# Kernel tuning notes

Hardware: AMD Instinct MI355X
Metric: run time of the kernel (lower is better)

## Reference

```python
import jax, jax.numpy as jnp
import numpy as np

N = 50000   # nodes
E = 600000  # edges (avg degree 12)
F = 16      # raw node features
P = 32      # n_channels_preproc
C = 128     # n_channels
L = 6       # n_gnn_layers
LBL = 2     # n_labels


def _dense_init(k, fan_in, shape):
    return (jax.random.normal(k, shape, jnp.float32) / np.float32(np.sqrt(fan_in)))


def setup_inputs() -> dict:
    key = jax.random.key(0)
    ks = jax.random.split(key, 12)
    return {
        "x": jax.random.normal(ks[0], (N, F), jnp.float32),
        "edge_src": jax.random.randint(ks[1], (E,), 0, N, dtype=jnp.int32),
        "edge_dst": jax.random.randint(ks[2], (E,), 0, N, dtype=jnp.int32),
        "edge_weight": jax.random.uniform(ks[3], (E,), jnp.float32),  # normalized-adjacency values
        "preproc_W": _dense_init(ks[4], F, (F, P)), "preproc_b": jnp.zeros((P,), jnp.float32),
        "fc_in1_W": _dense_init(ks[5], P, (P, C)), "fc_in1_b": jnp.zeros((C,), jnp.float32),
        "fc_in2_W": _dense_init(ks[6], P, (P, C)), "fc_in2_b": jnp.zeros((C,), jnp.float32),
        "gcn_W": _dense_init(ks[7], C, (L, C, C)), "gcn_b": jnp.zeros((L, C), jnp.float32),
        "fcg_W": _dense_init(ks[8], 2 * C, (L, 2 * C, C)), "fcg_b": jnp.zeros((L, C), jnp.float32),
        "last1_W": _dense_init(ks[9], 2 * C, (2 * C, C)), "last1_b": jnp.zeros((C,), jnp.float32),
        "last2_W": _dense_init(ks[10], C, (C, LBL)), "last2_b": jnp.zeros((LBL,), jnp.float32),
    }


def reference(x, edge_src, edge_dst, edge_weight,
              preproc_W, preproc_b, fc_in1_W, fc_in1_b, fc_in2_W, fc_in2_b,
              gcn_W, gcn_b, fcg_W, fcg_b, last1_W, last1_b, last2_W, last2_b):
    relu = jax.nn.relu
    h = relu(x @ preproc_W + preproc_b)                      # preproc Dense
    node_id = relu(h @ fc_in1_W + fc_in1_b)                  # node identity branch
    h = relu(h @ fc_in2_W + fc_in2_b)

    def layer(h, params):
        W, b, Wf, bf = params
        # GCNConv: act(A_hat @ (h @ W) + b), A_hat as COO edge list
        hw = h @ W                                           # [N, C]
        msg = hw[edge_src] * edge_weight[:, None]            # [E, C]
        agg = jax.ops.segment_sum(msg, edge_dst, num_segments=N)
        g = relu(agg + b)
        merged = jnp.concatenate([node_id, g], axis=-1)      # [N, 2C]
        return relu(merged @ Wf + bf), None                  # dropout = identity (eval)

    h, _ = jax.lax.scan(layer, h, (gcn_W, gcn_b, fcg_W, fcg_b))

    merged = jnp.concatenate([node_id, h], axis=-1)
    h = relu(merged @ last1_W + last1_b)
    return jax.nn.sigmoid(h @ last2_W + last2_b)             # [N, n_labels]
```

## Files before the change

### kernel.cpp

```cpp
#include <hip/hip_runtime.h>
#include <cstddef>
#include <cstdint>

#define NN 50000
#define NE 600000
#define NB 391

typedef __attribute__((ext_vector_type(8))) short bf16x8;
typedef __attribute__((ext_vector_type(4))) float f32x4;

#define SWZ(x) (((x) ^ ((x) >> 2)) & 3)

#define GLDS16(src, dst)                                                     \
    __builtin_amdgcn_global_load_lds(                                        \
        (const __attribute__((address_space(1))) void*)(src),                \
        (__attribute__((address_space(3))) void*)(dst), 16, 0, 0)

__device__ __forceinline__ float bf2f(ushort u) {
    return __uint_as_float(((uint32_t)u) << 16);
}
__device__ __forceinline__ ushort f2bf(float f) {
    uint32_t b = __float_as_uint(f);
    return (ushort)((b + 0x7FFF + ((b >> 16) & 1)) >> 16);
}

__global__ __launch_bounds__(256)
void convbh_kernel(const float* __restrict__ f1W, const float* __restrict__ f2W,
                   const float* __restrict__ gW, const float* __restrict__ fgW,
                   const float* __restrict__ l1W, ushort* __restrict__ wt,
                   const int* __restrict__ dst, int* __restrict__ bcnt)
{
    if (blockIdx.x < 1312) {
        int i = blockIdx.x * 256 + threadIdx.x;
        if (i >= 335872) return;
        float v;
        if (i < 4096) {
            int c = i >> 5, k = i & 31;
            v = f1W[k * 128 + c];
        } else if (i < 8192) {
            int j = i - 4096; int c = j >> 5, k = j & 31;
            v = f2W[k * 128 + c];
        } else if (i < 8192 + 98304) {
            int j = i - 8192; int l = j >> 14, r = j & 16383;
            int c = r >> 7, k = r & 127;
            v = gW[l * 16384 + k * 128 + c];
        } else if (i < 8192 + 98304 + 196608) {
            int j = i - (8192 + 98304); int l = j >> 15, r = j & 32767;
            int c = r >> 8, k = r & 255;
            v = fgW[l * 32768 + k * 128 + c];
        } else {
            int j = i - (8192 + 98304 + 196608);
            int c = j >> 8, k = j & 255;
            v = l1W[k * 128 + c];
        }
        wt[i] = f2bf(v);
    } else {
        __shared__ int h[NB];
        int tx = threadIdx.x;
        for (int i = tx; i < NB; i += 256) h[i] = 0;
        __syncthreads();
        int e0 = (blockIdx.x - 1312) * 1024;
#pragma unroll
        for (int k = 0; k < 4; ++k) {
            int e = e0 + k * 256 + tx;
            if (e < NE) atomicAdd(&h[dst[e] >> 7], 1);
        }
        __syncthreads();
        for (int i = tx; i < NB; i += 256)
            if (h[i]) atomicAdd(&bcnt[i], h[i]);
    }
}

__global__ __launch_bounds__(512)
void bscan_kernel(const int* __restrict__ bcnt, int* __restrict__ bbase,
                  int* __restrict__ bcur)
{
    __shared__ int buf[512];
    int t = threadIdx.x;
    int v = (t < NB) ? bcnt[t] : 0;
    buf[t] = v;
    __syncthreads();
    for (int s = 1; s < 512; s <<= 1) {
        int u = (t >= s) ? buf[t - s] : 0;
        __syncthreads();
        buf[t] += u;
        __syncthreads();
    }
    if (t < NB) {
        int ex = buf[t] - v;
        bbase[t] = ex;
        bcur[t]  = ex;
    }
    if (t == 0) bbase[NB] = NE;
}

__global__ __launch_bounds__(256)
void pass1_kernel(const int* __restrict__ src, const int* __restrict__ dst,
                  const float* __restrict__ w, int* __restrict__ bcur,
                  unsigned int* __restrict__ stage_pk,
                  unsigned char* __restrict__ stage_dl)
{
    __shared__ int cnt[NB];
    __shared__ int gbase[NB];
    int tx = threadIdx.x;
    for (int i = tx; i < NB; i += 256) cnt[i] = 0;
    __syncthreads();
    int e0 = blockIdx.x * 1024;
    int myd[4], myrank[4];
    unsigned int mypk[4];
#pragma unroll
    for (int k = 0; k < 4; ++k) {
        int e = e0 + k * 256 + tx;
        if (e < NE) {
            int d = dst[e];
            myd[k]    = d;
            mypk[k]   = (unsigned int)src[e] | ((unsigned int)f2bf(w[e]) << 17);
            myrank[k] = atomicAdd(&cnt[d >> 7], 1);
        } else {
            myd[k] = -1;
        }
    }
    __syncthreads();
    for (int i = tx; i < NB; i += 256)
        gbase[i] = cnt[i] ? atomicAdd(&bcur[i], cnt[i]) : 0;
    __syncthreads();
#pragma unroll
    for (int k = 0; k < 4; ++k) {
        if (myd[k] >= 0) {
            int p = gbase[myd[k] >> 7] + myrank[k];
            stage_pk[p] = mypk[k];
            stage_dl[p] = (unsigned char)(myd[k] & 127);
        }
    }
}

__global__ __launch_bounds__(256)
void p2pre_kernel(const unsigned int* __restrict__ stage_pk,
                  const unsigned char* __restrict__ stage_dl,
                  const int* __restrict__ bbase,
                  unsigned int* __restrict__ esw, int* __restrict__ off,
                  const float* __restrict__ x, const float* __restrict__ preW,
                  const float* __restrict__ preb, ushort* __restrict__ h0b)
{
    if (blockIdx.x < NB) {
        __shared__ int h[128];
        __shared__ int lofs[128];
        int b    = blockIdx.x;
        int tx   = threadIdx.x;
        int base = bbase[b];
        int cnt  = bbase[b + 1] - base;
        if (tx < 128) h[tx] = 0;
        __syncthreads();
        for (int i = tx; i < cnt; i += 256)
            atomicAdd(&h[stage_dl[base + i]], 1);
        __syncthreads();
        if (tx == 0) {
            int run = 0;
            for (int i = 0; i < 128; ++i) { lofs[i] = run; run += h[i]; }
        }
        __syncthreads();
        int node0 = b * 128;
        if (tx < 128) {
            int n = node0 + tx;
            if (n < NN) off[n] = base + lofs[tx];
            h[tx] = 0;
        }
        if (b == NB - 1 && tx == 0) off[NN] = NE;
        __syncthreads();
        for (int i = tx; i < cnt; i += 256) {
            int d = stage_dl[base + i];
            int r = atomicAdd(&h[d], 1);
            esw[base + lofs[d] + r] = stage_pk[base + i];
        }
    } else {
        __shared__ float Wl[512];
        __shared__ float bl[32];
        int tx = threadIdx.x;
        Wl[tx]       = preW[tx];
        Wl[tx + 256] = preW[tx + 256];
        if (tx < 32) bl[tx] = preb[tx];
        __syncthreads();
        int n = (blockIdx.x - NB) * 256 + tx;
        if (n >= NN) return;
        float xr[16];
        const float4* xp = (const float4*)(x + (size_t)n * 16);
#pragma unroll
        for (int q = 0; q < 4; ++q) {
            float4 v = xp[q];
            xr[q*4+0]=v.x; xr[q*4+1]=v.y; xr[q*4+2]=v.z; xr[q*4+3]=v.w;
        }
        float acc[32];
#pragma unroll
        for (int c = 0; c < 32; ++c) acc[c] = bl[c];
#pragma unroll
        for (int k = 0; k < 16; ++k)
#pragma unroll
            for (int c = 0; c < 32; ++c)
                acc[c] = fmaf(xr[k], Wl[k*32+c], acc[c]);
        ushort4* op = (ushort4*)(h0b + (size_t)n * 32);
#pragma unroll
        for (int q = 0; q < 8; ++q) {
            ushort4 v;
            v.x = f2bf(fmaxf(acc[q*4+0], 0.f));
            v.y = f2bf(fmaxf(acc[q*4+1], 0.f));
            v.z = f2bf(fmaxf(acc[q*4+2], 0.f));
            v.w = f2bf(fmaxf(acc[q*4+3], 0.f));
            op[q] = v;
        }
    }
}

__global__ __launch_bounds__(128)
void fc1f0_kernel(const ushort* __restrict__ h0b,
                  const ushort* __restrict__ wf1, const float* __restrict__ f1b,
                  ushort* __restrict__ nidb,
                  const ushort* __restrict__ wf2, const float* __restrict__ f2b,
                  const ushort* __restrict__ wg, ushort* __restrict__ hwb)
{
    __shared__ ushort Atile[64 * 32];
    __shared__ ushort Btile[128 * 32];
    __shared__ ushort Xt[64 * 128];
    const int tx   = threadIdx.x;
    const int wave = tx >> 6;
    const int lane = tx & 63;
    const int rs  = lane >> 2;
    const int chn = (lane & 3) ^ SWZ(rs);
    const int m    = lane & 15;
    const int quad = lane >> 4;
    const int slot = quad ^ SWZ(m);

    if (blockIdx.x < 782) {
        const int bm = blockIdx.x * 64;
        f32x4 acc0[8], acc1[8];
#pragma unroll
        for (int t = 0; t < 8; ++t) {
            acc0[t] = (f32x4){0.f, 0.f, 0.f, 0.f};
            acc1[t] = (f32x4){0.f, 0.f, 0.f, 0.f};
        }
#pragma unroll
        for (int i = 0; i < 2; ++i) {
            int seg = wave + 2 * i;
            int row = seg * 16 + rs;
            int ar  = bm + row; if (ar >= NN) ar = NN - 1;
            GLDS16(h0b + (size_t)ar * 32 + chn * 8, Atile + seg * 512);
        }
#pragma unroll
        for (int i = 0; i < 4; ++i) {
            int seg = wave + 2 * i;
            int col = seg * 16 + rs;
            GLDS16(wf1 + (size_t)col * 32 + chn * 8, Btile + seg * 512);
        }
        __syncthreads();
        bf16x8 af0 = *(const bf16x8*)(Atile + (wave * 32 + m) * 32 + slot * 8);
        bf16x8 af1 = *(const bf16x8*)(Atile + (wave * 32 + 16 + m) * 32 + slot * 8);
#pragma unroll
        for (int t = 0; t < 8; ++t) {
            bf16x8 bfr = *(const bf16x8*)(Btile + (t * 16 + m) * 32 + slot * 8);
            acc0[t] = __builtin_amdgcn_mfma_f32_16x16x32_bf16(af0, bfr, acc0[t], 0, 0, 0);
            acc1[t] = __builtin_amdgcn_mfma_f32_16x16x32_bf16(af1, bfr, acc1[t], 0, 0, 0);
        }
        __syncthreads();
#pragma unroll
        for (int half = 0; half < 2; ++half) {
            const int orow0 = bm + wave * 32 + half * 16 + quad * 4;
#pragma unroll
            for (int t = 0; t < 8; ++t) {
                int col = t * 16 + m;
                float bb = f1b[col];
                f32x4 a = half ? acc1[t] : acc0[t];
#pragma unroll
                for (int r = 0; r < 4; ++r) {
                    int row = orow0 + r;
                    if (row < NN)
                        nidb[(size_t)row * 128 + col] = f2bf(fmaxf(a[r] + bb, 0.f));
                }
            }
        }
    } else {
        const int bm = (blockIdx.x - 782) * 64;
        f32x4 acc0[8], acc1[8];
#pragma unroll
        for (int t = 0; t < 8; ++t) {
            acc0[t] = (f32x4){0.f, 0.f, 0.f, 0.f};
            acc1[t] = (f32x4){0.f, 0.f, 0.f, 0.f};
        }
#pragma unroll
        for (int i = 0; i < 2; ++i) {
            int seg = wave + 2 * i;
            int row = seg * 16 + rs;
            int ar  = bm + row; if (ar >= NN) ar = NN - 1;
            GLDS16(h0b + (size_t)ar * 32 + chn * 8, Atile + seg * 512);
        }
#pragma unroll
        for (int i = 0; i < 4; ++i) {
            int seg = wave + 2 * i;
            int col = seg * 16 + rs;
            GLDS16(wf2 + (size_t)col * 32 + chn * 8, Btile + seg * 512);
        }
        __syncthreads();
        {
            bf16x8 af0 = *(const bf16x8*)(Atile + (wave * 32 + m) * 32 + slot * 8);
            bf16x8 af1 = *(const bf16x8*)(Atile + (wave * 32 + 16 + m) * 32 + slot * 8);
#pragma unroll
            for (int t = 0; t < 8; ++t) {
                bf16x8 bfr = *(const bf16x8*)(Btile + (t * 16 + m) * 32 + slot * 8);
                acc0[t] = __builtin_amdgcn_mfma_f32_16x16x32_bf16(af0, bfr, acc0[t], 0, 0, 0);
                acc1[t] = __builtin_amdgcn_mfma_f32_16x16x32_bf16(af1, bfr, acc1[t], 0, 0, 0);
            }
        }
        __syncthreads();
#pragma unroll
        for (int half = 0; half < 2; ++half) {
            int rbase = wave * 32 + half * 16 + quad * 4;
#pragma unroll
            for (int t = 0; t < 8; ++t) {
                int col = t * 16 + m;
                float bb = f2b[col];
                int c32 = col >> 5, within = col & 7, ks = (col >> 3) & 3;
                f32x4 a = half ? acc1[t] : acc0[t];
#pragma unroll
                for (int r = 0; r < 4; ++r) {
                    int row = rbase + r;
                    int pos = ks ^ SWZ(row & 15);
                    Xt[row * 128 + c32 * 32 + pos * 8 + within] =
                        f2bf(fmaxf(a[r] + bb, 0.f));
                }
            }
        }
#pragma unroll
        for (int t = 0; t < 8; ++t) {
            acc0[t] = (f32x4){0.f, 0.f, 0.f, 0.f};
            acc1[t] = (f32x4){0.f, 0.f, 0.f, 0.f};
        }
        __syncthreads();
        for (int c32 = 0; c32 < 4; ++c32) {
            int kk = c32 * 32;
#pragma unroll
            for (int i = 0; i < 4; ++i) {
                int seg = wave + 2 * i;
                int col = seg * 16 + rs;
                GLDS16(wg + (size_t)col * 128 + kk + chn * 8, Btile + seg * 512);
            }
            __syncthreads();
            bf16x8 af0 = *(const bf16x8*)(Xt + (wave * 32 + m) * 128 + kk + slot * 8);
            bf16x8 af1 = *(const bf16x8*)(Xt + (wave * 32 + 16 + m) * 128 + kk + slot * 8);
#pragma unroll
            for (int t = 0; t < 8; ++t) {
                bf16x8 bfr = *(const bf16x8*)(Btile + (t * 16 + m) * 32 + slot * 8);
                acc0[t] = __builtin_amdgcn_mfma_f32_16x16x32_bf16(af0, bfr, acc0[t], 0, 0, 0);
                acc1[t] = __builtin_amdgcn_mfma_f32_16x16x32_bf16(af1, bfr, acc1[t], 0, 0, 0);
            }
            __syncthreads();
        }
#pragma unroll
        for (int half = 0; half < 2; ++half) {
            const int orow0 = bm + wave * 32 + half * 16 + quad * 4;
#pragma unroll
            for (int t = 0; t < 8; ++t) {
                int col = t * 16 + m;
                f32x4 a = half ? acc1[t] : acc0[t];
#pragma unroll
                for (int r = 0; r < 4; ++r) {
                    int row = orow0 + r;
                    if (row < NN)
                        hwb[(size_t)row * 128 + col] = f2bf(a[r]);
                }
            }
        }
    }
}

__global__ __launch_bounds__(512, 4)
void gemm_gather(const ushort* __restrict__ hw,
                 const unsigned int* __restrict__ esw,
                 const int* __restrict__ off,
                 const float* __restrict__ gbias,
                 const ushort* __restrict__ nid,
                 const ushort* __restrict__ Wt,
                 const float* __restrict__ bias,
                 const ushort* __restrict__ Wg,
                 ushort* __restrict__ out_hw, int nrows)
{
    __shared__ ushort Atile[2 * 64 * 32];
    __shared__ ushort Btile[2 * 128 * 32];
    __shared__ ushort AggXt[64 * 128];
    const int tx   = threadIdx.x;
    const int wave = tx >> 6;
    const int lane = tx & 63;
    const int bm   = blockIdx.x * 64;
    const int g    = wave >> 1;
    const int h    = wave & 1;
    const int rs   = lane >> 2;
    const int chn  = (lane & 3) ^ SWZ(rs);
    const int m    = lane & 15;
    const int quad = lane >> 4;
    const int slot = quad ^ SWZ(m);

    const int ac  = wave >> 2, asg = wave & 3;
    int aar = bm + asg * 16 + rs; if (aar >= nrows) aar = nrows - 1;

    auto stageA = [&](int koff) {
        GLDS16(nid + (size_t)aar * 128 + koff + ac * 32 + chn * 8,
               Atile + ac * 2048 + asg * 512);
    };
    auto stageB = [&](const ushort* W, int ldk, int koff) {
#pragma unroll
        for (int i = 0; i < 2; ++i) {
            int col = wave * 16 + rs;
            GLDS16(W + (size_t)col * ldk + koff + i * 32 + chn * 8,
                   Btile + i * 4096 + wave * 512);
        }
    };

    f32x4 acc[4];
#pragma unroll
    for (int t = 0; t < 4; ++t) acc[t] = (f32x4){0.f, 0.f, 0.f, 0.f};

    auto mfmaA = [&]() {
#pragma unroll
        for (int c = 0; c < 2; ++c) {
            bf16x8 af = *(const bf16x8*)(Atile + c * 2048 + (g * 16 + m) * 32 + slot * 8);
#pragma unroll
            for (int t = 0; t < 4; ++t) {
                bf16x8 bfr = *(const bf16x8*)(Btile + c * 4096 + (h * 64 + t * 16 + m) * 32 + slot * 8);
                acc[t] = __builtin_amdgcn_mfma_f32_16x16x32_bf16(af, bfr, acc[t], 0, 0, 0);
            }
        }
    };
    auto mfmaX = [&](int x) {
        const int row = g * 16 + m, rx = (row & 1) << 5;
#pragma unroll
        for (int c = 0; c < 2; ++c) {
            bf16x8 af = *(const bf16x8*)(AggXt + row * 128 + (((x * 2 + c) * 32 + slot * 8) ^ rx));
#pragma unroll
            for (int t = 0; t < 4; ++t) {
                bf16x8 bfr = *(const bf16x8*)(Btile + c * 4096 + (h * 64 + t * 16 + m) * 32 + slot * 8);
                acc[t] = __builtin_amdgcn_mfma_f32_16x16x32_bf16(af, bfr, acc[t], 0, 0, 0);
            }
        }
    };

    stageA(0);
    stageB(Wt, 256, 0);

    {
        const int n0   = bm + wave * 8;
        const int nend = n0 + 8;
        int n    = n0;
        const int base = off[n0 < NN ? n0 : NN];
        const int end  = off[nend < NN ? nend : NN];
        int nb = (n < NN) ? off[n + 1] : 0x7fffffff;
        const ushort* hp = hw + lane * 2;
        const float g0 = gbias[lane * 2], g1 = gbias[lane * 2 + 1];
        float a0 = 0.f, a1 = 0.f;
        const int c32g = lane >> 4;
        const int ksg  = (lane >> 2) & 3;
        const int wth  = (2 * lane) & 7;
        for (int chunk = base; chunk < end; chunk += 64) {
            int idx = chunk + lane;
            int pk = (idx < end) ? (int)esw[idx] : 0;
            int cnt = end - chunk; if (cnt > 64) cnt = 64;
            int cnt16 = (cnt + 15) & ~15;
            for (int j = 0; j < cnt16; j += 16) {
                int pp[16];
                unsigned int rv[16];
#pragma unroll
                for (int k = 0; k < 16; ++k)
                    pp[k] = __builtin_amdgcn_readlane(pk, j + k);
#pragma unroll
                for (int k = 0; k < 16; ++k)
                    rv[k] = *(const unsigned int*)(hp + (size_t)(pp[k] & 0x1FFFF) * 128);
#pragma unroll
                for (int k = 0; k < 16; ++k) {
                    int e = chunk + j + k;
                    while (e == nb) {
                        int row = n - bm;
                        unsigned int o = (unsigned int)f2bf(fmaxf(a0 + g0, 0.f)) |
                                         ((unsigned int)f2bf(fmaxf(a1 + g1, 0.f)) << 16);
                        int pos = ksg ^ SWZ(row & 15);
                        *(unsigned int*)(AggXt + row * 128 +
                            ((c32g * 32 + pos * 8 + wth) ^ ((row & 1) << 5))) = o;
                        a0 = 0.f; a1 = 0.f;
                        ++n;
                        nb = (n < nend && n < NN) ? off[n + 1] : 0x7fffffff;
                    }
                    float w = bf2f((ushort)((unsigned int)pp[k] >> 17));
                    a0 = fmaf(bf2f((ushort)(rv[k] & 0xffff)), w, a0);
                    a1 = fmaf(bf2f((ushort)(rv[k] >> 16)),    w, a1);
                }
            }
        }
        while (n < nend) {
            int row = n - bm;
            unsigned int o = (unsigned int)f2bf(fmaxf(a0 + g0, 0.f)) |
                             ((unsigned int)f2bf(fmaxf(a1 + g1, 0.f)) << 16);
            int pos = ksg ^ SWZ(row & 15);
            *(unsigned int*)(AggXt + row * 128 +
                ((c32g * 32 + pos * 8 + wth) ^ ((row & 1) << 5))) = o;
            a0 = 0.f; a1 = 0.f;
            ++n;
        }
    }

    __syncthreads();
    mfmaA();
    __syncthreads();
    stageA(64); stageB(Wt, 256, 64);
    __syncthreads();
    mfmaA();
    __syncthreads();
    stageB(Wt, 256, 128);
    __syncthreads();
    mfmaX(0);
    __syncthreads();
    stageB(Wt, 256, 192);
    __syncthreads();
    mfmaX(1);
    __syncthreads();

    stageB(Wg, 128, 0);

    {
        int rbase = g * 16 + quad * 4;
#pragma unroll
        for (int t = 0; t < 4; ++t) {
            int col = h * 64 + t * 16 + m;
            float bb = bias[col];
            int c32 = col >> 5, within = col & 7, ks = (col >> 3) & 3;
#pragma unroll
            for (int r = 0; r < 4; ++r) {
                int row = rbase + r;
                int pos = ks ^ SWZ(row & 15);
                AggXt[row * 128 + ((c32 * 32 + pos * 8 + within) ^ ((row & 1) << 5))] =
                    f2bf(fmaxf(acc[t][r] + bb, 0.f));
            }
        }
    }
#pragma unroll
    for (int t = 0; t < 4; ++t) acc[t] = (f32x4){0.f, 0.f, 0.f, 0.f};
    __syncthreads();

    mfmaX(0);
    __syncthreads();
    stageB(Wg, 128, 64);
    __syncthreads();
    mfmaX(1);

    {
        const int orow0 = bm + g * 16 + quad * 4;
#pragma unroll
        for (int t = 0; t < 4; ++t) {
            int col = h * 64 + t * 16 + m;
#pragma unroll
            for (int r = 0; r < 4; ++r) {
                int row = orow0 + r;
                if (row < nrows)
                    out_hw[(size_t)row * 128 + col] = f2bf(acc[t][r]);
            }
        }
    }
}

__global__ __launch_bounds__(512, 4)
void gemm_last(const ushort* __restrict__ hw,
               const unsigned int* __restrict__ esw,
               const int* __restrict__ off,
               const float* __restrict__ gbias,
               const ushort* __restrict__ nid,
               const ushort* __restrict__ Wt, const float* __restrict__ bias5,
               const ushort* __restrict__ Wl1, const float* __restrict__ l1b,
               const float* __restrict__ l2W, const float* __restrict__ l2b,
               float* __restrict__ out, int nrows)
{
    __shared__ ushort Atile[2 * 64 * 32];
    __shared__ ushort Btile[2 * 128 * 32];
    __shared__ ushort AggXt[64 * 128];
    const int tx   = threadIdx.x;
    const int wave = tx >> 6;
    const int lane = tx & 63;
    const int bm   = blockIdx.x * 64;
    const int g    = wave >> 1;
    const int h    = wave & 1;
    const int rs   = lane >> 2;
    const int chn  = (lane & 3) ^ SWZ(rs);
    const int m    = lane & 15;
    const int quad = lane >> 4;
    const int slot = quad ^ SWZ(m);

    const int ac  = wave >> 2, asg = wave & 3;
    int aar = bm + asg * 16 + rs; if (aar >= nrows) aar = nrows - 1;

    auto stageA = [&](int koff) {
        GLDS16(nid + (size_t)aar * 128 + koff + ac * 32 + chn * 8,
               Atile + ac * 2048 + asg * 512);
    };
    auto stageB = [&](const ushort* W, int ldk, int koff) {
#pragma unroll
        for (int i = 0; i < 2; ++i) {
            int col = wave * 16 + rs;
            GLDS16(W + (size_t)col * ldk + koff + i * 32 + chn * 8,
                   Btile + i * 4096 + wave * 512);
        }
    };

    f32x4 acc[4];
#pragma unroll
    for (int t = 0; t < 4; ++t) acc[t] = (f32x4){0.f, 0.f, 0.f, 0.f};

    auto mfmaA = [&]() {
#pragma unroll
        for (int c = 0; c < 2; ++c) {
            bf16x8 af = *(const bf16x8*)(Atile + c * 2048 + (g * 16 + m) * 32 + slot * 8);
#pragma unroll
            for (int t = 0; t < 4; ++t) {
                bf16x8 bfr = *(const bf16x8*)(Btile + c * 4096 + (h * 64 + t * 16 + m) * 32 + slot * 8);
                acc[t] = __builtin_amdgcn_mfma_f32_16x16x32_bf16(af, bfr, acc[t], 0, 0, 0);
            }
        }
    };
    auto mfmaX = [&](int x) {
        const int row = g * 16 + m, rx = (row & 1) << 5;
#pragma unroll
        for (int c = 0; c < 2; ++c) {
            bf16x8 af = *(const bf16x8*)(AggXt + row * 128 + (((x * 2 + c) * 32 + slot * 8) ^ rx));
#pragma unroll
            for (int t = 0; t < 4; ++t) {
                bf16x8 bfr = *(const bf16x8*)(Btile + c * 4096 + (h * 64 + t * 16 + m) * 32 + slot * 8);
                acc[t] = __builtin_amdgcn_mfma_f32_16x16x32_bf16(af, bfr, acc[t], 0, 0, 0);
            }
        }
    };

    stageA(0);
    stageB(Wt, 256, 0);

    {
        const int n0   = bm + wave * 8;
        const int nend = n0 + 8;
        int n    = n0;
        const int base = off[n0 < NN ? n0 : NN];
        const int end  = off[nend < NN ? nend : NN];
        int nb = (n < NN) ? off[n + 1] : 0x7fffffff;
        const ushort* hp = hw + lane * 2;
        const float g0 = gbias[lane * 2], g1 = gbias[lane * 2 + 1];
        float a0 = 0.f, a1 = 0.f;
        const int c32g = lane >> 4;
        const int ksg  = (lane >> 2) & 3;
        const int wth  = (2 * lane) & 7;
        for (int chunk = base; chunk < end; chunk += 64) {
            int idx = chunk + lane;
            int pk = (idx < end) ? (int)esw[idx] : 0;
            int cnt = end - chunk; if (cnt > 64) cnt = 64;
            int cnt16 = (cnt + 15) & ~15;
            for (int j = 0; j < cnt16; j += 16) {
                int pp[16];
                unsigned int rv[16];
#pragma unroll
                for (int k = 0; k < 16; ++k)
                    pp[k] = __builtin_amdgcn_readlane(pk, j + k);
#pragma unroll
                for (int k = 0; k < 16; ++k)
                    rv[k] = *(const unsigned int*)(hp + (size_t)(pp[k] & 0x1FFFF) * 128);
#pragma unroll
                for (int k = 0; k < 16; ++k) {
                    int e = chunk + j + k;
                    while (e == nb) {
                        int row = n - bm;
                        unsigned int o = (unsigned int)f2bf(fmaxf(a0 + g0, 0.f)) |
                                         ((unsigned int)f2bf(fmaxf(a1 + g1, 0.f)) << 16);
                        int pos = ksg ^ SWZ(row & 15);
                        *(unsigned int*)(AggXt + row * 128 +
                            ((c32g * 32 + pos * 8 + wth) ^ ((row & 1) << 5))) = o;
                        a0 = 0.f; a1 = 0.f;
                        ++n;
                        nb = (n < nend && n < NN) ? off[n + 1] : 0x7fffffff;
                    }
                    float w = bf2f((ushort)((unsigned int)pp[k] >> 17));
                    a0 = fmaf(bf2f((ushort)(rv[k] & 0xffff)), w, a0);
                    a1 = fmaf(bf2f((ushort)(rv[k] >> 16)),    w, a1);
                }
            }
        }
        while (n < nend) {
            int row = n - bm;
            unsigned int o = (unsigned int)f2bf(fmaxf(a0 + g0, 0.f)) |
                             ((unsigned int)f2bf(fmaxf(a1 + g1, 0.f)) << 16);
            int pos = ksg ^ SWZ(row & 15);
            *(unsigned int*)(AggXt + row * 128 +
                ((c32g * 32 + pos * 8 + wth) ^ ((row & 1) << 5))) = o;
            a0 = 0.f; a1 = 0.f;
            ++n;
        }
    }

    __syncthreads();
    mfmaA();
    __syncthreads();
    stageA(64); stageB(Wt, 256, 64);
    __syncthreads();
    mfmaA();
    __syncthreads();
    stageB(Wt, 256, 128);
    __syncthreads();
    mfmaX(0);
    __syncthreads();
    stageB(Wt, 256, 192);
    __syncthreads();
    mfmaX(1);
    __syncthreads();

    stageA(0);
    stageB(Wl1, 256, 0);

    {
        int rbase = g * 16 + quad * 4;
#pragma unroll
        for (int t = 0; t < 4; ++t) {
            int col = h * 64 + t * 16 + m;
            float bb = bias5[col];
            int c32 = col >> 5, within = col & 7, ks = (col >> 3) & 3;
#pragma unroll
            for (int r = 0; r < 4; ++r) {
                int row = rbase + r;
                int pos = ks ^ SWZ(row & 15);
                AggXt[row * 128 + ((c32 * 32 + pos * 8 + within) ^ ((row & 1) << 5))] =
                    f2bf(fmaxf(acc[t][r] + bb, 0.f));
            }
        }
    }
#pragma unroll
    for (int t = 0; t < 4; ++t) acc[t] = (f32x4){0.f, 0.f, 0.f, 0.f};
    __syncthreads();

    mfmaA();
    __syncthreads();
    stageA(64); stageB(Wl1, 256, 64);
    __syncthreads();
    mfmaA();
    __syncthreads();
    stageB(Wl1, 256, 128);
    __syncthreads();
    mfmaX(0);
    __syncthreads();
    stageB(Wl1, 256, 192);
    __syncthreads();
    mfmaX(1);

    float bb[4];
#pragma unroll
    for (int t = 0; t < 4; ++t) bb[t] = l1b[h * 64 + t * 16 + m];
    float pr0[4], pr1[4];
#pragma unroll
    for (int r = 0; r < 4; ++r) {
        float p0 = 0.f, p1 = 0.f;
#pragma unroll
        for (int t = 0; t < 4; ++t) {
            int col = h * 64 + t * 16 + m;
            float v = fmaxf(acc[t][r] + bb[t], 0.f);
            p0 = fmaf(v, l2W[col * 2 + 0], p0);
            p1 = fmaf(v, l2W[col * 2 + 1], p1);
        }
#pragma unroll
        for (int mask = 1; mask < 16; mask <<= 1) {
            p0 += __shfl_xor(p0, mask);
            p1 += __shfl_xor(p1, mask);
        }
        pr0[r] = p0; pr1[r] = p1;
    }
    float* pbuf = (float*)Atile;
    if (h == 1 && m == 0) {
#pragma unroll
        for (int r = 0; r < 4; ++r) {
            int lrow = g * 16 + quad * 4 + r;
            pbuf[lrow * 2 + 0] = pr0[r];
            pbuf[lrow * 2 + 1] = pr1[r];
        }
    }
    __syncthreads();
    if (h == 0 && m == 0) {
        float b20 = l2b[0], b21 = l2b[1];
#pragma unroll
        for (int r = 0; r < 4; ++r) {
            int lrow = g * 16 + quad * 4 + r;
            int row = bm + lrow;
            if (row < nrows) {
                float p0 = pr0[r] + pbuf[lrow * 2 + 0] + b20;
                float p1 = pr1[r] + pbuf[lrow * 2 + 1] + b21;
                out[(size_t)row * 2 + 0] = 1.f / (1.f + __expf(-p0));
                out[(size_t)row * 2 + 1] = 1.f / (1.f + __expf(-p1));
            }
        }
    }
}

extern "C" void kernel_launch(void* const* d_in, const int* in_sizes, int n_in,
                              void* d_out, int out_size, void* d_ws, size_t ws_size,
                              hipStream_t stream)
{
    const float* x    = (const float*)d_in[0];
    const int*   esrc = (const int*)  d_in[1];
    const int*   edst = (const int*)  d_in[2];
    const float* ew   = (const float*)d_in[3];
    const float* preW = (const float*)d_in[4];
    const float* preb = (const float*)d_in[5];
    const float* f1W  = (const float*)d_in[6];
    const float* f1b  = (const float*)d_in[7];
    const float* f2W  = (const float*)d_in[8];
    const float* f2b  = (const float*)d_in[9];
    const float* gW   = (const float*)d_in[10];
    const float* gb   = (const float*)d_in[11];
    const float* fgW  = (const float*)d_in[12];
    const float* fgb  = (const float*)d_in[13];
    const float* l1W  = (const float*)d_in[14];
    const float* l1b  = (const float*)d_in[15];
    const float* l2W  = (const float*)d_in[16];
    const float* l2b  = (const float*)d_in[17];
    float* out = (float*)d_out;

    ushort* wt   = (ushort*)d_ws;
    ushort* wf1  = wt;
    ushort* wf2  = wf1 + 4096;
    ushort* wg   = wf2 + 4096;
    ushort* wfg  = wg  + 98304;
    ushort* wl1  = wfg + 196608;
    ushort* h0b  = wl1 + 32768;
    ushort* nidb = h0b  + (size_t)NN * 32;
    ushort* hwb  = nidb + (size_t)NN * 128;
    ushort* hwb2 = hwb  + (size_t)NN * 128;
    ushort* endu = hwb2 + (size_t)NN * 128;
    unsigned int* esw      = (unsigned int*)(((uintptr_t)endu + 15) & ~(uintptr_t)15);
    unsigned int* stage_pk = esw + NE;
    int*          bcnt     = (int*)(stage_pk + NE);
    int*          bbase    = bcnt + NB + 1;
    int*          bcur     = bbase + NB + 1;
    int*          off      = bcur + NB + 1;
    unsigned char* stage_dl = (unsigned char*)(off + NN + 2);

    const int gblocks = (NN + 63) / 64;
    const int eblocks = (NE + 1023) / 1024;

    hipMemsetAsync(bcnt, 0, (size_t)NB * sizeof(int), stream);
    convbh_kernel<<<1312 + eblocks, 256, 0, stream>>>(f1W, f2W, gW, fgW, l1W, wt,
                                                      edst, bcnt);
    bscan_kernel<<<1, 512, 0, stream>>>(bcnt, bbase, bcur);
    pass1_kernel<<<eblocks, 256, 0, stream>>>(esrc, edst, ew, bcur, stage_pk, stage_dl);
    p2pre_kernel<<<NB + (NN + 255) / 256, 256, 0, stream>>>(stage_pk, stage_dl, bbase,
                                                            esw, off, x, preW, preb, h0b);

    fc1f0_kernel<<<2 * gblocks, 128, 0, stream>>>(h0b, wf1, f1b, nidb,
                                                  wf2, f2b, wg, hwb);
    ushort* cur = hwb;
    ushort* nxt = hwb2;
    for (int l = 0; l < 5; ++l) {
        gemm_gather<<<gblocks, 512, 0, stream>>>(cur, esw, off,
                                                 gb + (size_t)l * 128, nidb,
                                                 wfg + (size_t)l * 32768,
                                                 fgb + (size_t)l * 128,
                                                 wg + (size_t)(l + 1) * 16384,
                                                 nxt, NN);
        ushort* tmp = cur; cur = nxt; nxt = tmp;
    }
    gemm_last<<<gblocks, 512, 0, stream>>>(cur, esw, off,
                                           gb + (size_t)5 * 128, nidb,
                                           wfg + (size_t)5 * 32768,
                                           fgb + (size_t)5 * 128,
                                           wl1, l1b, l2W, l2b, out, NN);
}
```

Before: 409.3 us.

## Double-buffer GEMM K-tiles with vmcnt waits and prefetch gather rows

Changes the fused gather+GEMM kernels from single-stage 64-wide K tiles with full __syncthreads around each step to 32-wide K tiles in two LDS buffers. The next tile's global-to-LDS copy is issued before the MFMAs on the current tile, with explicit s_waitcnt vmcnt/lgkmcnt and raw s_barrier plus sched_barrier, so load latency overlaps compute. The first 128 edges of each wave's gather are software-pipelined, issuing the next 16 row loads before accumulating the current 16. It also drops the occupancy hint from launch_bounds, so register pressure and the correctness of the manual wait counts become risks.

```diff
diff --git a/kernel.cpp b/kernel.cpp
--- a/kernel.cpp
+++ b/kernel.cpp
@@ -15,6 +15,14 @@
     __builtin_amdgcn_global_load_lds(                                        \
         (const __attribute__((address_space(1))) void*)(src),                \
         (__attribute__((address_space(3))) void*)(dst), 16, 0, 0)
+
+#define SBAR() do { __builtin_amdgcn_sched_barrier(0);                        \
+                    __builtin_amdgcn_s_barrier();                             \
+                    __builtin_amdgcn_sched_barrier(0); } while (0)
+#define WVM(N) do { asm volatile("s_waitcnt vmcnt(" #N ")" ::: "memory");     \
+                    __builtin_amdgcn_sched_barrier(0); } while (0)
+#define WLG()  do { asm volatile("s_waitcnt lgkmcnt(0)" ::: "memory");        \
+                    __builtin_amdgcn_sched_barrier(0); } while (0)
 
 __device__ __forceinline__ float bf2f(ushort u) {
     return __uint_as_float(((uint32_t)u) << 16);
@@ -370,7 +378,7 @@
     }
 }
 
-__global__ __launch_bounds__(512, 4)
+__global__ __launch_bounds__(512)
 void gemm_gather(const ushort* __restrict__ hw,
                  const unsigned int* __restrict__ esw,
                  const int* __restrict__ off,
@@ -381,8 +389,8 @@
                  const ushort* __restrict__ Wg,
                  ushort* __restrict__ out_hw, int nrows)
 {
-    __shared__ ushort Atile[2 * 64 * 32];
-    __shared__ ushort Btile[2 * 128 * 32];
+    __shared__ ushort Atile[2][64 * 32];
+    __shared__ ushort Btile[2][128 * 32];
     __shared__ ushort AggXt[64 * 128];
     const int tx   = threadIdx.x;
     const int wave = tx >> 6;
@@ -396,52 +404,40 @@
     const int quad = lane >> 4;
     const int slot = quad ^ SWZ(m);
 
-    const int ac  = wave >> 2, asg = wave & 3;
-    int aar = bm + asg * 16 + rs; if (aar >= nrows) aar = nrows - 1;
-
-    auto stageA = [&](int koff) {
-        GLDS16(nid + (size_t)aar * 128 + koff + ac * 32 + chn * 8,
-               Atile + ac * 2048 + asg * 512);
+    int aar = bm + wave * 16 + rs; if (aar >= nrows) aar = nrows - 1;
+
+    auto stA = [&](int koff, int buf) {
+        if (wave < 4)
+            GLDS16(nid + (size_t)aar * 128 + koff + chn * 8, Atile[buf] + wave * 512);
     };
-    auto stageB = [&](const ushort* W, int ldk, int koff) {
-#pragma unroll
-        for (int i = 0; i < 2; ++i) {
-            int col = wave * 16 + rs;
-            GLDS16(W + (size_t)col * ldk + koff + i * 32 + chn * 8,
-                   Btile + i * 4096 + wave * 512);
-        }
+    auto stB = [&](const ushort* W, int ldk, int koff, int buf) {
+        int col = wave * 16 + rs;
+        GLDS16(W + (size_t)col * ldk + koff + chn * 8, Btile[buf] + wave * 512);
     };
 
     f32x4 acc[4];
 #pragma unroll
     for (int t = 0; t < 4; ++t) acc[t] = (f32x4){0.f, 0.f, 0.f, 0.f};
 
-    auto mfmaA = [&]() {
-#pragma unroll
-        for (int c = 0; c < 2; ++c) {
-            bf16x8 af = *(const bf16x8*)(Atile + c * 2048 + (g * 16 + m) * 32 + slot * 8);
-#pragma unroll
-            for (int t = 0; t < 4; ++t) {
-                bf16x8 bfr = *(const bf16x8*)(Btile + c * 4096 + (h * 64 + t * 16 + m) * 32 + slot * 8);
-                acc[t] = __builtin_amdgcn_mfma_f32_16x16x32_bf16(af, bfr, acc[t], 0, 0, 0);
-            }
+    auto mmA = [&](int buf) {
+        bf16x8 af = *(const bf16x8*)(Atile[buf] + (g * 16 + m) * 32 + slot * 8);
+#pragma unroll
+        for (int t = 0; t < 4; ++t) {
+            bf16x8 bfr = *(const bf16x8*)(Btile[buf] + (h * 64 + t * 16 + m) * 32 + slot * 8);
+            acc[t] = __builtin_amdgcn_mfma_f32_16x16x32_bf16(af, bfr, acc[t], 0, 0, 0);
         }
     };
-    auto mfmaX = [&](int x) {
+    auto mmX = [&](int kb, int buf) {
         const int row = g * 16 + m, rx = (row & 1) << 5;
-#pragma unroll
-        for (int c = 0; c < 2; ++c) {
-            bf16x8 af = *(const bf16x8*)(AggXt + row * 128 + (((x * 2 + c) * 32 + slot * 8) ^ rx));
-#pragma unroll
-            for (int t = 0; t < 4; ++t) {
-                bf16x8 bfr = *(const bf16x8*)(Btile + c * 4096 + (h * 64 + t * 16 + m) * 32 + slot * 8);
-                acc[t] = __builtin_amdgcn_mfma_f32_16x16x32_bf16(af, bfr, acc[t], 0, 0, 0);
-            }
+        bf16x8 af = *(const bf16x8*)(AggXt + row * 128 + ((kb * 32 + slot * 8) ^ rx));
+#pragma unroll
+        for (int t = 0; t < 4; ++t) {
+            bf16x8 bfr = *(const bf16x8*)(Btile[buf] + (h * 64 + t * 16 + m) * 32 + slot * 8);
+            acc[t] = __builtin_amdgcn_mfma_f32_16x16x32_bf16(af, bfr, acc[t], 0, 0, 0);
         }
     };
 
-    stageA(0);
-    stageB(Wt, 256, 0);
+    stA(0, 0); stB(Wt, 256, 0, 0);
 
     {
         const int n0   = bm + wave * 8;
@@ -456,7 +452,65 @@
         const int c32g = lane >> 4;
         const int ksg  = (lane >> 2) & 3;
         const int wth  = (2 * lane) & 7;
-        for (int chunk = base; chunk < end; chunk += 64) {
+
+        auto flushTo = [&](int e) {
+            while (e == nb) {
+                int row = n - bm;
+                unsigned int o = (unsigned int)f2bf(fmaxf(a0 + g0, 0.f)) |
+                                 ((unsigned int)f2bf(fmaxf(a1 + g1, 0.f)) << 16);
+                int pos = ksg ^ SWZ(row & 15);
+                *(unsigned int*)(AggXt + row * 128 +
+                    ((c32g * 32 + pos * 8 + wth) ^ ((row & 1) << 5))) = o;
+                a0 = 0.f; a1 = 0.f;
+                ++n;
+                nb = (n < nend && n < NN) ? off[n + 1] : 0x7fffffff;
+            }
+        };
+
+        const int total = end - base;
+        const int lim   = total < 128 ? total : 128;
+        int pk0 = (base + lane < end)      ? (int)esw[base + lane]      : 0;
+        int pk1 = (base + 64 + lane < end) ? (int)esw[base + 64 + lane] : 0;
+
+        unsigned int rvA[16], rvB[16];
+        auto issueB16 = [&](int b, unsigned int* rv) {
+            int pkw = (b < 4) ? pk0 : pk1;
+            int jo  = (b & 3) * 16;
+#pragma unroll
+            for (int k = 0; k < 16; ++k) {
+                int pp = __builtin_amdgcn_readlane(pkw, jo + k);
+                rv[k] = *(const unsigned int*)(hp + (size_t)(pp & 0x1FFFF) * 128);
+            }
+        };
+        auto procB16 = [&](int b, const unsigned int* rv) {
+            int pkw = (b < 4) ? pk0 : pk1;
+            int jo  = (b & 3) * 16;
+            int eb  = base + b * 16;
+#pragma unroll
+            for (int k = 0; k < 16; ++k) {
+                int e = eb + k;
+                if (e >= end) break;
+                flushTo(e);
+                int pp = __builtin_amdgcn_readlane(pkw, jo + k);
+                float w = bf2f((ushort)((unsigned int)pp >> 17));
+                a0 = fmaf(bf2f((ushort)(rv[k] & 0xffffu)), w, a0);
+                a1 = fmaf(bf2f((ushort)(rv[k] >> 16)), w, a1);
+            }
+        };
+
+        if (lim > 0) {
+            issueB16(0, rvA);
+            int b = 0;
+            for (;;) {
+                if ((b + 1) * 16 < lim) issueB16(b + 1, rvB);
+                procB16(b, rvA);
+                ++b; if (b * 16 >= lim) break;
+                if ((b + 1) * 16 < lim) issueB16(b + 1, rvA);
+                procB16(b, rvB);
+                ++b; if (b * 16 >= lim) break;
+            }
+        }
+        for (int chunk = base + 128; chunk < end; chunk += 64) {
             int idx = chunk + lane;
             int pk = (idx < end) ? (int)esw[idx] : 0;
             int cnt = end - chunk; if (cnt > 64) cnt = 64;
@@ -473,17 +527,8 @@
 #pragma unroll
                 for (int k = 0; k < 16; ++k) {
                     int e = chunk + j + k;
-                    while (e == nb) {
-                        int row = n - bm;
-                        unsigned int o = (unsigned int)f2bf(fmaxf(a0 + g0, 0.f)) |
-                                         ((unsigned int)f2bf(fmaxf(a1 + g1, 0.f)) << 16);
-                        int pos = ksg ^ SWZ(row & 15);
-                        *(unsigned int*)(AggXt + row * 128 +
-                            ((c32g * 32 + pos * 8 + wth) ^ ((row & 1) << 5))) = o;
-                        a0 = 0.f; a1 = 0.f;
-                        ++n;
-                        nb = (n < nend && n < NN) ? off[n + 1] : 0x7fffffff;
-                    }
+                    if (e >= end) break;
+                    flushTo(e);
                     float w = bf2f((ushort)((unsigned int)pp[k] >> 17));
                     a0 = fmaf(bf2f((ushort)(rv[k] & 0xffff)), w, a0);
                     a1 = fmaf(bf2f((ushort)(rv[k] >> 16)),    w, a1);
@@ -503,23 +548,23 @@
     }
 
     __syncthreads();
-    mfmaA();
-    __syncthreads();
-    stageA(64); stageB(Wt, 256, 64);
-    __syncthreads();
-    mfmaA();
-    __syncthreads();
-    stageB(Wt, 256, 128);
-    __syncthreads();
-    mfmaX(0);
-    __syncthreads();
-    stageB(Wt, 256, 192);
-    __syncthreads();
-    mfmaX(1);
-    __syncthreads();
-
-    stageB(Wg, 128, 0);
-
+
+    stA(32, 1); stB(Wt, 256, 32, 1);
+    if (wave < 4) { WVM(2); } else { WVM(1); }
+    SBAR(); mmA(0); WLG(); SBAR();
+    stA(64, 0); stB(Wt, 256, 64, 0);
+    if (wave < 4) { WVM(2); } else { WVM(1); }
+    SBAR(); mmA(1); WLG(); SBAR();
+    stA(96, 1); stB(Wt, 256, 96, 1);
+    if (wave < 4) { WVM(2); } else { WVM(1); }
+    SBAR(); mmA(0); WLG(); SBAR();
+    stB(Wt, 256, 128, 0); WVM(1); SBAR(); mmA(1);    WLG(); SBAR();
+    stB(Wt, 256, 160, 1); WVM(1); SBAR(); mmX(0, 0); WLG(); SBAR();
+    stB(Wt, 256, 192, 0); WVM(1); SBAR(); mmX(1, 1); WLG(); SBAR();
+    stB(Wt, 256, 224, 1); WVM(1); SBAR(); mmX(2, 0); WLG(); SBAR();
+                          WVM(0); SBAR(); mmX(3, 1); WLG(); SBAR();
+
+    stB(Wg, 128, 0, 0);
     {
         int rbase = g * 16 + quad * 4;
 #pragma unroll
@@ -538,13 +583,12 @@
     }
 #pragma unroll
     for (int t = 0; t < 4; ++t) acc[t] = (f32x4){0.f, 0.f, 0.f, 0.f};
-    __syncthreads();
-
-    mfmaX(0);
-    __syncthreads();
-    stageB(Wg, 128, 64);
-    __syncthreads();
-    mfmaX(1);
+    WLG(); SBAR();
+
+    stB(Wg, 128, 32, 1); WVM(1); SBAR(); mmX(0, 0); WLG(); SBAR();
+    stB(Wg, 128, 64, 0); WVM(1); SBAR(); mmX(1, 1); WLG(); SBAR();
+    stB(Wg, 128, 96, 1); WVM(1); SBAR(); mmX(2, 0); WLG(); SBAR();
+                         WVM(0); SBAR(); mmX(3, 1);
 
     {
         const int orow0 = bm + g * 16 + quad * 4;
@@ -561,7 +605,7 @@
     }
 }
 
-__global__ __launch_bounds__(512, 4)
+__global__ __launch_bounds__(512)
 void gemm_last(const ushort* __restrict__ hw,
                const unsigned int* __restrict__ esw,
                const int* __restrict__ off,
@@ -572,8 +616,8 @@
                const float* __restrict__ l2W, const float* __restrict__ l2b,
                float* __restrict__ out, int nrows)
 {
-    __shared__ ushort Atile[2 * 64 * 32];
-    __shared__ ushort Btile[2 * 128 * 32];
+    __shared__ ushort Atile[2][64 * 32];
+    __shared__ ushort Btile[2][128 * 32];
     __shared__ ushort AggXt[64 * 128];
     const int tx   = threadIdx.x;
     const int wave = tx >> 6;
@@ -587,52 +631,40 @@
     const int quad = lane >> 4;
     const int slot = quad ^ SWZ(m);
 
-    const int ac  = wave >> 2, asg = wave & 3;
-    int aar = bm + asg * 16 + rs; if (aar >= nrows) aar = nrows - 1;
-
-    auto stageA = [&](int koff) {
-        GLDS16(nid + (size_t)aar * 128 + koff + ac * 32 + chn * 8,
-               Atile + ac * 2048 + asg * 512);
+    int aar = bm + wave * 16 + rs; if (aar >= nrows) aar = nrows - 1;
+
+    auto stA = [&](int koff, int buf) {
+        if (wave < 4)
+            GLDS16(nid + (size_t)aar * 128 + koff + chn * 8, Atile[buf] + wave * 512);
     };
-    auto stageB = [&](const ushort* W, int ldk, int koff) {
-#pragma unroll
-        for (int i = 0; i < 2; ++i) {
-            int col = wave * 16 + rs;
-            GLDS16(W + (size_t)col * ldk + koff + i * 32 + chn * 8,
-                   Btile + i * 4096 + wave * 512);
-        }
+    auto stB = [&](const ushort* W, int ldk, int koff, int buf) {
+        int col = wave * 16 + rs;
+        GLDS16(W + (size_t)col * ldk + koff + chn * 8, Btile[buf] + wave * 512);
     };
 
     f32x4 acc[4];
 #pragma unroll
     for (int t = 0; t < 4; ++t) acc[t] = (f32x4){0.f, 0.f, 0.f, 0.f};
 
-    auto mfmaA = [&]() {
-#pragma unroll
-        for (int c = 0; c < 2; ++c) {
-            bf16x8 af = *(const bf16x8*)(Atile + c * 2048 + (g * 16 + m) * 32 + slot * 8);
-#pragma unroll
-            for (int t = 0; t < 4; ++t) {
-                bf16x8 bfr = *(const bf16x8*)(Btile + c * 4096 + (h * 64 + t * 16 + m) * 32 + slot * 8);
-                acc[t] = __builtin_amdgcn_mfma_f32_16x16x32_bf16(af, bfr, acc[t], 0, 0, 0);
-            }
+    auto mmA = [&](int buf) {
+        bf16x8 af = *(const bf16x8*)(Atile[buf] + (g * 16 + m) * 32 + slot * 8);
+#pragma unroll
+        for (int t = 0; t < 4; ++t) {
+            bf16x8 bfr = *(const bf16x8*)(Btile[buf] + (h * 64 + t * 16 + m) * 32 + slot * 8);
+            acc[t] = __builtin_amdgcn_mfma_f32_16x16x32_bf16(af, bfr, acc[t], 0, 0, 0);
         }
     };
-    auto mfmaX = [&](int x) {
+    auto mmX = [&](int kb, int buf) {
         const int row = g * 16 + m, rx = (row & 1) << 5;
-#pragma unroll
-        for (int c = 0; c < 2; ++c) {
-            bf16x8 af = *(const bf16x8*)(AggXt + row * 128 + (((x * 2 + c) * 32 + slot * 8) ^ rx));
-#pragma unroll
-            for (int t = 0; t < 4; ++t) {
-                bf16x8 bfr = *(const bf16x8*)(Btile + c * 4096 + (h * 64 + t * 16 + m) * 32 + slot * 8);
-                acc[t] = __builtin_amdgcn_mfma_f32_16x16x32_bf16(af, bfr, acc[t], 0, 0, 0);
-            }
+        bf16x8 af = *(const bf16x8*)(AggXt + row * 128 + ((kb * 32 + slot * 8) ^ rx));
+#pragma unroll
+        for (int t = 0; t < 4; ++t) {
+            bf16x8 bfr = *(const bf16x8*)(Btile[buf] + (h * 64 + t * 16 + m) * 32 + slot * 8);
+            acc[t] = __builtin_amdgcn_mfma_f32_16x16x32_bf16(af, bfr, acc[t], 0, 0, 0);
         }
     };
 
-    stageA(0);
-    stageB(Wt, 256, 0);
+    stA(0, 0); stB(Wt, 256, 0, 0);
 
     {
         const int n0   = bm + wave * 8;
@@ -647,7 +679,65 @@
         const int c32g = lane >> 4;
         const int ksg  = (lane >> 2) & 3;
         const int wth  = (2 * lane) & 7;
-        for (int chunk = base; chunk < end; chunk += 64) {
+
+        auto flushTo = [&](int e) {
+            while (e == nb) {
+                int row = n - bm;
+                unsigned int o = (unsigned int)f2bf(fmaxf(a0 + g0, 0.f)) |
+                                 ((unsigned int)f2bf(fmaxf(a1 + g1, 0.f)) << 16);
+                int pos = ksg ^ SWZ(row & 15);
+                *(unsigned int*)(AggXt + row * 128 +
+                    ((c32g * 32 + pos * 8 + wth) ^ ((row & 1) << 5))) = o;
+                a0 = 0.f; a1 = 0.f;
+                ++n;
+                nb = (n < nend && n < NN) ? off[n + 1] : 0x7fffffff;
+            }
+        };
+
+        const int total = end - base;
+        const int lim   = total < 128 ? total : 128;
+        int pk0 = (base + lane < end)      ? (int)esw[base + lane]      : 0;
+        int pk1 = (base + 64 + lane < end) ? (int)esw[base + 64 + lane] : 0;
+
+        unsigned int rvA[16], rvB[16];
+        auto issueB16 = [&](int b, unsigned int* rv) {
+            int pkw = (b < 4) ? pk0 : pk1;
+            int jo  = (b & 3) * 16;
+#pragma unroll
+            for (int k = 0; k < 16; ++k) {
+                int pp = __builtin_amdgcn_readlane(pkw, jo + k);
+                rv[k] = *(const unsigned int*)(hp + (size_t)(pp & 0x1FFFF) * 128);
+            }
+        };
+        auto procB16 = [&](int b, const unsigned int* rv) {
+            int pkw = (b < 4) ? pk0 : pk1;
+            int jo  = (b & 3) * 16;
+            int eb  = base + b * 16;
+#pragma unroll
+            for (int k = 0; k < 16; ++k) {
+                int e = eb + k;
+                if (e >= end) break;
+                flushTo(e);
+                int pp = __builtin_amdgcn_readlane(pkw, jo + k);
+                float w = bf2f((ushort)((unsigned int)pp >> 17));
+                a0 = fmaf(bf2f((ushort)(rv[k] & 0xffffu)), w, a0);
+                a1 = fmaf(bf2f((ushort)(rv[k] >> 16)), w, a1);
+            }
+        };
+
+        if (lim > 0) {
+            issueB16(0, rvA);
+            int b = 0;
+            for (;;) {
+                if ((b + 1) * 16 < lim) issueB16(b + 1, rvB);
+                procB16(b, rvA);
+                ++b; if (b * 16 >= lim) break;
+                if ((b + 1) * 16 < lim) issueB16(b + 1, rvA);
+                procB16(b, rvB);
+                ++b; if (b * 16 >= lim) break;
+            }
+        }
+        for (int chunk = base + 128; chunk < end; chunk += 64) {
             int idx = chunk + lane;
             int pk = (idx < end) ? (int)esw[idx] : 0;
             int cnt = end - chunk; if (cnt > 64) cnt = 64;
@@ -664,17 +754,8 @@
 #pragma unroll
                 for (int k = 0; k < 16; ++k) {
                     int e = chunk + j + k;
-                    while (e == nb) {
-                        int row = n - bm;
-                        unsigned int o = (unsigned int)f2bf(fmaxf(a0 + g0, 0.f)) |
-                                         ((unsigned int)f2bf(fmaxf(a1 + g1, 0.f)) << 16);
-                        int pos = ksg ^ SWZ(row & 15);
-                        *(unsigned int*)(AggXt + row * 128 +
-                            ((c32g * 32 + pos * 8 + wth) ^ ((row & 1) << 5))) = o;
-                        a0 = 0.f; a1 = 0.f;
-                        ++n;
-                        nb = (n < nend && n < NN) ? off[n + 1] : 0x7fffffff;
-                    }
+                    if (e >= end) break;
+                    flushTo(e);
                     float w = bf2f((ushort)((unsigned int)pp[k] >> 17));
                     a0 = fmaf(bf2f((ushort)(rv[k] & 0xffff)), w, a0);
                     a1 = fmaf(bf2f((ushort)(rv[k] >> 16)),    w, a1);
@@ -694,24 +775,23 @@
     }
 
     __syncthreads();
-    mfmaA();
-    __syncthreads();
-    stageA(64); stageB(Wt, 256, 64);
-    __syncthreads();
-    mfmaA();
-    __syncthreads();
-    stageB(Wt, 256, 128);
-    __syncthreads();
-    mfmaX(0);
-    __syncthreads();
-    stageB(Wt, 256, 192);
-    __syncthreads();
-    mfmaX(1);
-    __syncthreads();
-
-    stageA(0);
-    stageB(Wl1, 256, 0);
-
+
+    stA(32, 1); stB(Wt, 256, 32, 1);
+    if (wave < 4) { WVM(2); } else { WVM(1); }
+    SBAR(); mmA(0); WLG(); SBAR();
+    stA(64, 0); stB(Wt, 256, 64, 0);
+    if (wave < 4) { WVM(2); } else { WVM(1); }
+    SBAR(); mmA(1); WLG(); SBAR();
+    stA(96, 1); stB(Wt, 256, 96, 1);
+    if (wave < 4) { WVM(2); } else { WVM(1); }
+    SBAR(); mmA(0); WLG(); SBAR();
+    stB(Wt, 256, 128, 0); WVM(1); SBAR(); mmA(1);    WLG(); SBAR();
+    stB(Wt, 256, 160, 1); WVM(1); SBAR(); mmX(0, 0); WLG(); SBAR();
+    stB(Wt, 256, 192, 0); WVM(1); SBAR(); mmX(1, 1); WLG(); SBAR();
+    stB(Wt, 256, 224, 1); WVM(1); SBAR(); mmX(2, 0); WLG(); SBAR();
+                          WVM(0); SBAR(); mmX(3, 1); WLG(); SBAR();
+
+    stA(0, 0); stB(Wl1, 256, 0, 0);
     {
         int rbase = g * 16 + quad * 4;
 #pragma unroll
@@ -730,21 +810,22 @@
     }
 #pragma unroll
     for (int t = 0; t < 4; ++t) acc[t] = (f32x4){0.f, 0.f, 0.f, 0.f};
-    __syncthreads();
-
-    mfmaA();
-    __syncthreads();
-    stageA(64); stageB(Wl1, 256, 64);
-    __syncthreads();
-    mfmaA();
-    __syncthreads();
-    stageB(Wl1, 256, 128);
-    __syncthreads();
-    mfmaX(0);
-    __syncthreads();
-    stageB(Wl1, 256, 192);
-    __syncthreads();
-    mfmaX(1);
+    WLG(); SBAR();
+
+    stA(32, 1); stB(Wl1, 256, 32, 1);
+    if (wave < 4) { WVM(2); } else { WVM(1); }
+    SBAR(); mmA(0); WLG(); SBAR();
+    stA(64, 0); stB(Wl1, 256, 64, 0);
+    if (wave < 4) { WVM(2); } else { WVM(1); }
+    SBAR(); mmA(1); WLG(); SBAR();
+    stA(96, 1); stB(Wl1, 256, 96, 1);
+    if (wave < 4) { WVM(2); } else { WVM(1); }
+    SBAR(); mmA(0); WLG(); SBAR();
+    stB(Wl1, 256, 128, 0); WVM(1); SBAR(); mmA(1);    WLG(); SBAR();
+    stB(Wl1, 256, 160, 1); WVM(1); SBAR(); mmX(0, 0); WLG(); SBAR();
+    stB(Wl1, 256, 192, 0); WVM(1); SBAR(); mmX(1, 1); WLG(); SBAR();
+    stB(Wl1, 256, 224, 1); WVM(1); SBAR(); mmX(2, 0); WLG(); SBAR();
+                           WVM(0); SBAR(); mmX(3, 1);
 
     float bb[4];
 #pragma unroll
```

After: 464.6 us. 1.13x slower.
